# Performance work log

Hardware: AMD Instinct MI355X
Metric: run time of the kernel (lower is better)

## Reference

```python
import jax, jax.numpy as jnp
import numpy as np

E = 200000      # n_edges
IN = 128        # input_nf
HID = 32        # hidden_nf
H = 4           # att_heads
OUT = 128       # output_nf
MAXK = 16       # MAX_K neighbor slots


def setup_inputs() -> dict:
    key = jax.random.key(0)
    ks = jax.random.split(key, 12)
    Z = jax.random.normal(ks[0], (E, IN), dtype=jnp.float32)
    idx = jax.random.randint(ks[1], (E, 2, MAXK), 0, E)
    red = jax.random.uniform(ks[2], (E, 1, MAXK)) < 0.15
    klist = jnp.where(red, -1, idx).astype(jnp.int64)
    s = 0.05  # xavier-ish scale
    Wq = jax.random.normal(ks[3], (H, HID, IN), dtype=jnp.float32) * s
    Wk = jax.random.normal(ks[4], (H, HID, IN), dtype=jnp.float32) * s
    Wv = jax.random.normal(ks[5], (H, HID, IN), dtype=jnp.float32) * s
    Wb = jax.random.normal(ks[6], (H, 1, IN), dtype=jnp.float32) * s
    Wg = jax.random.normal(ks[7], (H, HID, IN), dtype=jnp.float32) * s
    bg = jnp.zeros((H, HID), dtype=jnp.float32)
    Wout = jax.random.normal(ks[8], (OUT, H * HID), dtype=jnp.float32) * s
    bout = jnp.zeros((OUT,), dtype=jnp.float32)
    return {"Z": Z, "klist": klist, "Wq": Wq, "Wk": Wk, "Wv": Wv,
            "Wb": Wb, "Wg": Wg, "bg": bg, "Wout": Wout, "bout": bout}


def reference(Z, klist, Wq, Wk, Wv, Wb, Wg, bg, Wout, bout):
    idx_i, idx_j = klist[:, 0], klist[:, 1]          # (E, K)
    red = idx_i == -1
    valid = (~red).astype(Z.dtype)[..., None]        # (E, K, 1)
    ii = jnp.where(red, 0, idx_i)
    jj = jnp.where(red, 0, idx_j)
    scale = 1.0 / np.sqrt(HID)
    outs = []
    for h in range(H):  # att_heads: small fixed loop over structurally distinct heads
        q = Z @ Wq[h].T                              # (E, HID)
        k = Z @ Wk[h].T
        v = Z @ Wv[h].T
        b = (Z @ Wb[h].T)[:, 0]                      # (E,)
        g = jax.nn.sigmoid(Z @ Wg[h].T + bg[h])      # (E, HID)
        tri_k = jnp.take(k, ii, axis=0) * valid      # (E, K, HID), redundant slots zeroed
        tri_v = jnp.take(v, ii, axis=0) * valid
        tri_b = jnp.take(b, jj, axis=0) * valid[..., 0]  # (E, K)
        scores = scale * jnp.einsum('eh,ekh->ek', q, tri_k) + tri_b
        alpha = jax.nn.softmax(scores, axis=1)       # (E, K)
        att = jnp.einsum('ek,ekh->eh', alpha, tri_v) # (E, HID)
        outs.append(g * att)
    out = jnp.concatenate(outs, axis=-1) @ Wout.T + bout  # (E, OUT)
    # dropout is identity in eval mode
    return out
```

## Files before the change

### kernel.cpp

```cpp
#include <hip/hip_runtime.h>
#include <hip/hip_bf16.h>
#include <stdint.h>

#define EDGES 200000
#define INF   128
#define HID   32
#define NHEAD 4
#define OUTF  128
#define MAXK  16

#define NPAD  528

#define XPAD  136

typedef unsigned short u16;
typedef __attribute__((ext_vector_type(8))) short bf16x8;
typedef __attribute__((ext_vector_type(4))) float f32x4;

__device__ __forceinline__ u16 f2bf(float f) {
  union { float f; uint32_t u; } v; v.f = f;
  uint32_t u = v.u;
  return (u16)((u + 0x7FFFu + ((u >> 16) & 1u)) >> 16);
}
__device__ __forceinline__ float bflo(uint32_t p) {
  union { uint32_t u; float f; } v; v.u = p << 16;
  return v.f;
}
__device__ __forceinline__ float bfhi(uint32_t p) {
  union { uint32_t u; float f; } v; v.u = p & 0xFFFF0000u;
  return v.f;
}

__device__ __forceinline__ uint32_t cvtpk_bf16(float lo, float hi) {
  float2 t; t.x = lo; t.y = hi;
  __hip_bfloat162 h = __float22bfloat162_rn(t);
  uint32_t u;
  __builtin_memcpy(&u, &h, 4);
  return u;
}
__device__ __forceinline__ bf16x8 pack8(float4 f0, float4 f1) {
  union { uint32_t u[4]; bf16x8 v; } r;
  r.u[0] = cvtpk_bf16(f0.x, f0.y);
  r.u[1] = cvtpk_bf16(f0.z, f0.w);
  r.u[2] = cvtpk_bf16(f1.x, f1.y);
  r.u[3] = cvtpk_bf16(f1.z, f1.w);
  return r.v;
}
__device__ __forceinline__ float sigm(float x) {
  return 1.0f / (1.0f + __expf(-x));
}

template <int CTRL>
__device__ __forceinline__ float dpp_add(float x) {
  int y = __builtin_amdgcn_update_dpp(0, __builtin_bit_cast(int, x),
                                      CTRL, 0xF, 0xF, true);
  return x + __builtin_bit_cast(float, y);
}
__device__ __forceinline__ float row16_sum(float x) {
  x = dpp_add<0xB1>(x);
  x = dpp_add<0x4E>(x);
  x = dpp_add<0x141>(x);
  x = dpp_add<0x140>(x);
  return x;
}

struct AccPair { f32x4 a, b; };
__device__ __forceinline__ AccPair tile_mm(const u16* __restrict__ W, int row0,
                                           int ml, int blk,
                                           const bf16x8 (&zfr)[2][4], int ldw) {
  bf16x8 wfr[4];
#pragma unroll
  for (int kk = 0; kk < 4; ++kk)
    wfr[kk] = *(const bf16x8*)(W + (size_t)(row0 + ml) * ldw + kk * 32 + blk * 8);
  AccPair r;
  r.a = (f32x4){0.f, 0.f, 0.f, 0.f};
  r.b = (f32x4){0.f, 0.f, 0.f, 0.f};
#pragma unroll
  for (int kk = 0; kk < 4; ++kk) {
    r.a = __builtin_amdgcn_mfma_f32_16x16x32_bf16(wfr[kk], zfr[0][kk], r.a, 0, 0, 0);
    r.b = __builtin_amdgcn_mfma_f32_16x16x32_bf16(wfr[kk], zfr[1][kk], r.b, 0, 0, 0);
  }
  return r;
}

__device__ __forceinline__ void load_zfr(const float* __restrict__ Z, long e0,
                                         int ml, int blk, bf16x8 (&zfr)[2][4]) {
#pragma unroll
  for (int s = 0; s < 2; ++s) {
    const float* zp = Z + (e0 + s * 16 + ml) * INF + blk * 8;
#pragma unroll
    for (int kk = 0; kk < 4; ++kk) {
      float4 f0 = *(const float4*)(zp + kk * 32);
      float4 f1 = *(const float4*)(zp + kk * 32 + 4);
      zfr[s][kk] = pack8(f0, f1);
    }
  }
}

__device__ __forceinline__ void ds_stage_pair(u16* sb, int ml, int blk, int t,
                                              uint2 pa, uint2 pb) {
  const int col2 = (t * 16 + blk * 4) * 2;
  const int swz = (ml & 7) << 4;
  *(uint2*)((char*)sb + ((ml * 128 + col2) ^ swz)) = pa;
  *(uint2*)((char*)sb + (((16 + ml) * 128 + col2) ^ swz)) = pb;
}
__device__ __forceinline__ void flush_group(const u16* sb, int lane,
                                            u16* __restrict__ dst, long e0,
                                            int rowu16, int colu16) {
  const int rr = lane >> 3;
  const int c8 = (lane & 7) * 8;
#pragma unroll
  for (int i = 0; i < 4; ++i) {
    const int row = i * 8 + rr;
    bf16x8 v = *(const bf16x8*)((const char*)sb +
                                ((row * 128 + c8 * 2) ^ ((row & 7) << 4)));
    *(bf16x8*)(dst + (e0 + row) * rowu16 + colu16 + c8) = v;
  }
}

__global__ __launch_bounds__(256) void prep_kernel(
    const float* __restrict__ Wq, const float* __restrict__ Wk,
    const float* __restrict__ Wv, const float* __restrict__ Wb,
    const float* __restrict__ Wg, const float* __restrict__ Wout,
    u16* __restrict__ Wc, u16* __restrict__ Woutb)
{
  int t = blockIdx.x * 256 + threadIdx.x;
  if (t < NPAD * INF) {
    int n = t >> 7, k = t & 127;
    float v = 0.0f;
    if (n < 128)       v = Wq[n * 128 + k];
    else if (n < 256)  v = Wg[(n - 128) * 128 + k];
    else if (n < 512) {
      int m = n - 256, h = m >> 6, c = m & 63;
      v = (c < 32) ? Wk[(h * 32 + c) * 128 + k] : Wv[(h * 32 + (c - 32)) * 128 + k];
    } else if (n < 516) v = Wb[(n - 512) * 128 + k];
    Wc[t] = f2bf(v);
  } else if (t < NPAD * INF + OUTF * 128) {
    int u = t - NPAD * INF;
    Woutb[u] = f2bf(Wout[u]);
  }
}

__global__ __launch_bounds__(256) void proj_kernel(
    const float* __restrict__ Z, const u16* __restrict__ Wc,
    u16* __restrict__ kvb, float* __restrict__ bb)
{
  __shared__ u16 stage[4][2][2048];

  const int wid = threadIdx.x >> 6, lane = threadIdx.x & 63;
  const int ml = lane & 15, blk = lane >> 4;
  const long e0 = (long)blockIdx.x * 128 + wid * 32;
  if (e0 >= EDGES) return;

  bf16x8 zfr[2][4];
  load_zfr(Z, e0, ml, blk, zfr);

  for (int g = 0; g < 4; ++g) {
    u16* sb = stage[wid][g & 1];
#pragma unroll
    for (int t = 0; t < 4; ++t) {
      AccPair acc = tile_mm(Wc, 256 + (g * 4 + t) * 16, ml, blk, zfr, INF);
      uint2 pa, pb;
      pa.x = cvtpk_bf16(acc.a[0], acc.a[1]); pa.y = cvtpk_bf16(acc.a[2], acc.a[3]);
      pb.x = cvtpk_bf16(acc.b[0], acc.b[1]); pb.y = cvtpk_bf16(acc.b[2], acc.b[3]);
      ds_stage_pair(sb, ml, blk, t, pa, pb);
    }
    flush_group(sb, lane, kvb, e0, 256, g * 64);
  }

  {
    AccPair acc = tile_mm(Wc, 512, ml, blk, zfr, INF);
    if (blk == 0) {
      *(float4*)(bb + (e0 + ml) * 4) =
          make_float4(acc.a[0], acc.a[1], acc.a[2], acc.a[3]);
      *(float4*)(bb + (e0 + 16 + ml) * 4) =
          make_float4(acc.b[0], acc.b[1], acc.b[2], acc.b[3]);
    }
  }
}

__global__ __launch_bounds__(256) void attn_out_kernel(
    const float* __restrict__ Z, const u16* __restrict__ Wc,
    const float* __restrict__ bg,
    const int* __restrict__ klist, const u16* __restrict__ kvb,
    const float* __restrict__ bb, const u16* __restrict__ Woutb,
    const float* __restrict__ bout, float* __restrict__ out)
{
  __shared__ u16 qs[32 * XPAD];
  __shared__ u16 gs[32 * XPAD];
  __shared__ u16 xs[32 * XPAD];

  const int wid = threadIdx.x >> 6;
  const int lane = threadIdx.x & 63;
  const long e0 = (long)blockIdx.x * 32;
  const int ml = lane & 15, blk = lane >> 4;

  {
    bf16x8 zfr[2][4];
    load_zfr(Z, e0, ml, blk, zfr);

#pragma unroll
    for (int t = 0; t < 2; ++t) {
      const int nt = wid * 2 + t;
      AccPair acc = tile_mm(Wc, nt * 16, ml, blk, zfr, INF);
      const int n0 = nt * 16 + blk * 4;
      uint2 pa, pb;
      pa.x = cvtpk_bf16(acc.a[0], acc.a[1]); pa.y = cvtpk_bf16(acc.a[2], acc.a[3]);
      pb.x = cvtpk_bf16(acc.b[0], acc.b[1]); pb.y = cvtpk_bf16(acc.b[2], acc.b[3]);
      *(uint2*)(&qs[ml * XPAD + n0]) = pa;
      *(uint2*)(&qs[(16 + ml) * XPAD + n0]) = pb;
    }
#pragma unroll
    for (int t = 0; t < 2; ++t) {
      const int nt = wid * 2 + t;
      AccPair acc = tile_mm(Wc, 128 + nt * 16, ml, blk, zfr, INF);
      const int n0 = nt * 16 + blk * 4;
      float4 b4 = *(const float4*)(bg + n0);
      uint2 pa, pb;
      pa.x = cvtpk_bf16(sigm(acc.a[0] + b4.x), sigm(acc.a[1] + b4.y));
      pa.y = cvtpk_bf16(sigm(acc.a[2] + b4.z), sigm(acc.a[3] + b4.w));
      pb.x = cvtpk_bf16(sigm(acc.b[0] + b4.x), sigm(acc.b[1] + b4.y));
      pb.y = cvtpk_bf16(sigm(acc.b[2] + b4.z), sigm(acc.b[3] + b4.w));
      *(uint2*)(&gs[ml * XPAD + n0]) = pa;
      *(uint2*)(&gs[(16 + ml) * XPAD + n0]) = pb;
    }
  }
  __syncthreads();

  const int h = lane >> 4;
  const int kvo = h * 64 + (lane & 15) * 2;
  const float scale = 0.17677669529663687f;

#pragma unroll 1
  for (int it = 0; it < 8; ++it) {
    const int le = wid * 8 + it;
    int e = (int)e0 + le;
    e = __builtin_amdgcn_readfirstlane(e);

    const uint32_t q2 = *(const uint32_t*)(&qs[le * XPAD + 2 * lane]);
    const uint32_t g2 = *(const uint32_t*)(&gs[le * XPAD + 2 * lane]);
    const float q0 = bflo(q2), q1 = bfhi(q2);

    float sc[MAXK];
    uint32_t vvm[MAXK];
    const int* kl = klist + (size_t)e * 32;
#pragma unroll
    for (int nb = 0; nb < MAXK; ++nb) {
      const int ii = kl[nb];
      const int jj = kl[16 + nb];
      const bool valid = (ii >= 0);
      const int is = valid ? ii : 0;
      const int js = valid ? jj : 0;
      const u16* kvrow = kvb + (size_t)is * 256;
      uint32_t kki = *(const uint32_t*)(kvrow + kvo);
      uint32_t vvi = *(const uint32_t*)(kvrow + kvo + 32);
      float p = q0 * bflo(kki) + q1 * bfhi(kki);
      p = row16_sum(p);
      float bj = bb[(size_t)js * 4 + h];
      sc[nb]  = valid ? (scale * p + bj) : 0.0f;
      vvm[nb] = valid ? vvi : 0u;
    }

    float m = sc[0];
#pragma unroll
    for (int nb = 1; nb < MAXK; ++nb) m = fmaxf(m, sc[nb]);
    float s = 0.f, a0 = 0.f, a1 = 0.f;
#pragma unroll
    for (int nb = 0; nb < MAXK; ++nb) {
      float al = __expf(sc[nb] - m);
      s += al;
      a0 += al * bflo(vvm[nb]);
      a1 += al * bfhi(vvm[nb]);
    }
    float inv = 1.0f / s;
    uint32_t xo = cvtpk_bf16(bflo(g2) * a0 * inv, bfhi(g2) * a1 * inv);
    *(uint32_t*)(&xs[le * XPAD + 2 * lane]) = xo;
  }

  __syncthreads();

  bf16x8 xfr[2][4];
#pragma unroll
  for (int s = 0; s < 2; ++s) {
#pragma unroll
    for (int kk = 0; kk < 4; ++kk)
      xfr[s][kk] = *(const bf16x8*)(&xs[(s * 16 + ml) * XPAD + kk * 32 + blk * 8]);
  }

  const long eA = e0 + ml, eB = e0 + 16 + ml;

#pragma unroll
  for (int t = 0; t < 2; ++t) {
    const int nt = wid * 2 + t;
    AccPair acc = tile_mm(Woutb, nt * 16, ml, blk, xfr, 128);
    const int o0 = nt * 16 + blk * 4;
    float4 b4 = *(const float4*)(bout + o0);
    float4 ra = make_float4(acc.a[0] + b4.x, acc.a[1] + b4.y,
                            acc.a[2] + b4.z, acc.a[3] + b4.w);
    float4 rb = make_float4(acc.b[0] + b4.x, acc.b[1] + b4.y,
                            acc.b[2] + b4.z, acc.b[3] + b4.w);
    *(float4*)(out + eA * 128 + o0) = ra;
    *(float4*)(out + eB * 128 + o0) = rb;
  }
}

extern "C" void kernel_launch(void* const* d_in, const int* in_sizes, int n_in,
                              void* d_out, int out_size, void* d_ws, size_t ws_size,
                              hipStream_t stream) {
  const float* Z     = (const float*)d_in[0];
  const int*   klist = (const int*)  d_in[1];
  const float* Wq    = (const float*)d_in[2];
  const float* Wk    = (const float*)d_in[3];
  const float* Wv    = (const float*)d_in[4];
  const float* Wb    = (const float*)d_in[5];
  const float* Wg    = (const float*)d_in[6];
  const float* bg    = (const float*)d_in[7];
  const float* Wout  = (const float*)d_in[8];
  const float* bout  = (const float*)d_in[9];
  float* out = (float*)d_out;

  char* ws = (char*)d_ws;
  u16*   Wc    = (u16*)(ws);
  u16*   Woutb = (u16*)(ws + 135168);
  u16*   kvb   = (u16*)(ws + 167936);
  float* bb    = (float*)(ws + 102567936);

  prep_kernel<<<(NPAD * INF + OUTF * 128 + 255) / 256, 256, 0, stream>>>(
      Wq, Wk, Wv, Wb, Wg, Wout, Wc, Woutb);
  proj_kernel<<<(EDGES + 127) / 128, 256, 0, stream>>>(
      Z, Wc, kvb, bb);
  attn_out_kernel<<<EDGES / 32, 256, 0, stream>>>(
      Z, Wc, bg, klist, kvb, bb, Woutb, bout, out);
}
```

Measured before the change: 516.6 us.

## Process two edges per wavefront in attention gather with 8-byte loads

The attention loop now handles two edges per wavefront: each lane owns four hidden channels, and 8 lanes cover one head. Loads from the KV table widen from 4 to 8 bytes, the dot-product reduction drops one DPP step, and the loop trip count halves. This doubles the neighbor gathers in flight per wave and gives each lane more independent work. The proj kernel's double-buffered staging is also reduced to a single buffer to cut LDS use, which may expose write/read hazards between groups.

```diff
diff --git a/kernel.cpp b/kernel.cpp
--- a/kernel.cpp
+++ b/kernel.cpp
@@ -56,11 +56,10 @@
                                       CTRL, 0xF, 0xF, true);
   return x + __builtin_bit_cast(float, y);
 }
-__device__ __forceinline__ float row16_sum(float x) {
+__device__ __forceinline__ float row8_sum(float x) {
   x = dpp_add<0xB1>(x);
   x = dpp_add<0x4E>(x);
   x = dpp_add<0x141>(x);
-  x = dpp_add<0x140>(x);
   return x;
 }
 
@@ -145,7 +144,7 @@
     const float* __restrict__ Z, const u16* __restrict__ Wc,
     u16* __restrict__ kvb, float* __restrict__ bb)
 {
-  __shared__ u16 stage[4][2][2048];
+  __shared__ u16 stage[4][2048];
 
   const int wid = threadIdx.x >> 6, lane = threadIdx.x & 63;
   const int ml = lane & 15, blk = lane >> 4;
@@ -156,7 +155,7 @@
   load_zfr(Z, e0, ml, blk, zfr);
 
   for (int g = 0; g < 4; ++g) {
-    u16* sb = stage[wid][g & 1];
+    u16* sb = stage[wid];
 #pragma unroll
     for (int t = 0; t < 4; ++t) {
       AccPair acc = tile_mm(Wc, 256 + (g * 4 + t) * 16, ml, blk, zfr, INF);
@@ -227,22 +226,25 @@
   }
   __syncthreads();
 
-  const int h = lane >> 4;
-  const int kvo = h * 64 + (lane & 15) * 2;
+  const int eh = lane >> 5;
+  const int h  = (lane >> 3) & 3;
+  const int l  = lane & 7;
+  const int kvo = h * 64 + l * 4;
+  const int qgo = h * 32 + l * 4;
   const float scale = 0.17677669529663687f;
 
 #pragma unroll 1
-  for (int it = 0; it < 8; ++it) {
-    const int le = wid * 8 + it;
-    int e = (int)e0 + le;
-    e = __builtin_amdgcn_readfirstlane(e);
-
-    const uint32_t q2 = *(const uint32_t*)(&qs[le * XPAD + 2 * lane]);
-    const uint32_t g2 = *(const uint32_t*)(&gs[le * XPAD + 2 * lane]);
-    const float q0 = bflo(q2), q1 = bfhi(q2);
+  for (int it = 0; it < 4; ++it) {
+    const int le = wid * 8 + it * 2 + eh;
+    const int e  = (int)e0 + le;
+
+    const uint2 q4 = *(const uint2*)(&qs[le * XPAD + qgo]);
+    const uint2 g4 = *(const uint2*)(&gs[le * XPAD + qgo]);
+    const float q0 = bflo(q4.x), q1 = bfhi(q4.x);
+    const float q2 = bflo(q4.y), q3 = bfhi(q4.y);
 
     float sc[MAXK];
-    uint32_t vvm[MAXK];
+    uint2 vvm[MAXK];
     const int* kl = klist + (size_t)e * 32;
 #pragma unroll
     for (int nb = 0; nb < MAXK; ++nb) {
@@ -252,29 +254,34 @@
       const int is = valid ? ii : 0;
       const int js = valid ? jj : 0;
       const u16* kvrow = kvb + (size_t)is * 256;
-      uint32_t kki = *(const uint32_t*)(kvrow + kvo);
-      uint32_t vvi = *(const uint32_t*)(kvrow + kvo + 32);
-      float p = q0 * bflo(kki) + q1 * bfhi(kki);
-      p = row16_sum(p);
+      uint2 kk4 = *(const uint2*)(kvrow + kvo);
+      uint2 vv4 = *(const uint2*)(kvrow + kvo + 32);
+      float p = q0 * bflo(kk4.x) + q1 * bfhi(kk4.x)
+              + q2 * bflo(kk4.y) + q3 * bfhi(kk4.y);
+      p = row8_sum(p);
       float bj = bb[(size_t)js * 4 + h];
-      sc[nb]  = valid ? (scale * p + bj) : 0.0f;
-      vvm[nb] = valid ? vvi : 0u;
+      sc[nb]   = valid ? (scale * p + bj) : 0.0f;
+      vvm[nb]  = valid ? vv4 : make_uint2(0u, 0u);
     }
 
     float m = sc[0];
 #pragma unroll
     for (int nb = 1; nb < MAXK; ++nb) m = fmaxf(m, sc[nb]);
-    float s = 0.f, a0 = 0.f, a1 = 0.f;
+    float s = 0.f, a0 = 0.f, a1 = 0.f, a2 = 0.f, a3 = 0.f;
 #pragma unroll
     for (int nb = 0; nb < MAXK; ++nb) {
       float al = __expf(sc[nb] - m);
       s += al;
-      a0 += al * bflo(vvm[nb]);
-      a1 += al * bfhi(vvm[nb]);
+      a0 += al * bflo(vvm[nb].x);
+      a1 += al * bfhi(vvm[nb].x);
+      a2 += al * bflo(vvm[nb].y);
+      a3 += al * bfhi(vvm[nb].y);
     }
     float inv = 1.0f / s;
-    uint32_t xo = cvtpk_bf16(bflo(g2) * a0 * inv, bfhi(g2) * a1 * inv);
-    *(uint32_t*)(&xs[le * XPAD + 2 * lane]) = xo;
+    uint2 xo;
+    xo.x = cvtpk_bf16(bflo(g4.x) * a0 * inv, bfhi(g4.x) * a1 * inv);
+    xo.y = cvtpk_bf16(bflo(g4.y) * a2 * inv, bfhi(g4.y) * a3 * inv);
+    *(uint2*)(&xs[le * XPAD + qgo]) = xo;
   }
 
   __syncthreads();
```

Result: slower. 650.8 us (+26.0%).
